# Kernel optimization log

Hardware: AMD Instinct MI355X
Metric: run time of the kernel (lower is better)

## Reference

```python
import jax, jax.numpy as jnp
import numpy as np

B = 65536          # batch
E = 512            # embedding_dim
SL = 128           # speed_latent_dim
H = 256            # hidden_size
NB = 6             # num_branch
D = E + SL         # 640, branch input dim


def _linear_init(k, din, dout):
    bound = 1.0 / np.sqrt(din)
    kw, kb = jax.random.split(k)
    W = jax.random.uniform(kw, (din, dout), minval=-bound, maxval=bound, dtype=jnp.float32)
    b = jax.random.uniform(kb, (dout,), minval=-bound, maxval=bound, dtype=jnp.float32)
    return W, b


def setup_inputs() -> dict:
    key = jax.random.key(0)
    ks = jax.random.split(key, 10)
    embedding = jax.random.normal(ks[0], (B, E), dtype=jnp.float32)
    speed = jax.random.uniform(ks[1], (B, 1), dtype=jnp.float32)
    command = jax.random.randint(ks[2], (B,), 1, NB + 1)  # values in 1..6

    # speed_in: Linear(1,H) -> ReLU -> Linear(H,SL)
    si_W1, si_b1 = _linear_init(ks[3], 1, H)
    si_W2, si_b2 = _linear_init(ks[4], H, SL)

    # speed_out: Linear(D,H) -> ReLU -> Linear(H,H) -> ReLU -> Linear(H,1)
    so_W1, so_b1 = _linear_init(ks[5], D, H)
    so_W2, so_b2 = _linear_init(ks[6], H, H)
    so_W3, so_b3 = _linear_init(ks[7], H, 1)

    # NB branches, each Linear(D,H)->ReLU->Linear(H,H)->ReLU->Linear(H,3)->Sigmoid
    def mk_branch(k):
        k1, k2, k3 = jax.random.split(k, 3)
        W1, b1 = _linear_init(k1, D, H)
        W2, b2 = _linear_init(k2, H, H)
        W3, b3 = _linear_init(k3, H, 3)
        return W1, b1, W2, b2, W3, b3

    bW1, bb1, bW2, bb2, bW3, bb3 = jax.vmap(mk_branch)(jax.random.split(ks[8], NB))

    return {
        "embedding": embedding, "speed": speed, "command": command,
        "si_W1": si_W1, "si_b1": si_b1, "si_W2": si_W2, "si_b2": si_b2,
        "bW1": bW1, "bb1": bb1, "bW2": bW2, "bb2": bb2, "bW3": bW3, "bb3": bb3,
        "so_W1": so_W1, "so_b1": so_b1, "so_W2": so_W2, "so_b2": so_b2,
        "so_W3": so_W3, "so_b3": so_b3,
    }


def reference(embedding, speed, command,
              si_W1, si_b1, si_W2, si_b2,
              bW1, bb1, bW2, bb2, bW3, bb3,
              so_W1, so_b1, so_W2, so_b2, so_W3, so_b3):
    # speed_in MLP and concat
    s = jax.nn.relu(speed @ si_W1 + si_b1) @ si_W2 + si_b2          # [B, SL]
    emb = jnp.concatenate([embedding, s], axis=1)                    # [B, D]

    # all branches computed densely (as in the torch module), then one-hot mask
    h1 = jax.nn.relu(jnp.einsum('bd,ndh->nbh', emb, bW1) + bb1[:, None, :])   # [NB,B,H]
    h2 = jax.nn.relu(jnp.einsum('nbh,nhk->nbk', h1, bW2) + bb2[:, None, :])   # [NB,B,H]
    out = jax.nn.sigmoid(jnp.einsum('nbk,nko->nbo', h2, bW3) + bb3[:, None, :])  # [NB,B,3]

    mask = (jnp.arange(NB)[:, None] == (command - 1)[None, :]).astype(out.dtype)  # [NB,B]
    control_pred = jnp.sum(out * mask[:, :, None], axis=0)           # [B, 3]

    # speed prediction head
    sp = jax.nn.relu(emb @ so_W1 + so_b1)
    sp = jax.nn.relu(sp @ so_W2 + so_b2)
    speed_pred = sp @ so_W3 + so_b3                                  # [B, 1]

    return control_pred, speed_pred
```

## Files before the change

### kernel.cpp

```cpp
#include <hip/hip_runtime.h>
#include <cstdint>
#include <cstddef>

typedef _Float16 f16;
typedef f16 f16x8 __attribute__((ext_vector_type(8)));
typedef float f32x4 __attribute__((ext_vector_type(4)));

#define B_ROWS 65536
#define NT_BRANCH 1030
#define NT_SPEED 1024

constexpr size_t OFF_SF16   = 0;
constexpr size_t SZ_SF16    = (size_t)B_ROWS * 128 * 2;
constexpr size_t OFF_SIW2T  = OFF_SF16 + SZ_SF16;
constexpr size_t SZ_SIW2T   = (size_t)128 * 256 * 2;
constexpr size_t OFF_BW1T   = OFF_SIW2T + SZ_SIW2T;
constexpr size_t SZ_BW1T    = (size_t)6 * 256 * 640 * 2;
constexpr size_t OFF_BW2T   = OFF_BW1T + SZ_BW1T;
constexpr size_t SZ_BW2T    = (size_t)6 * 256 * 256 * 2;
constexpr size_t OFF_SOW1T  = OFF_BW2T + SZ_BW2T;
constexpr size_t SZ_SOW1T   = (size_t)256 * 640 * 2;
constexpr size_t OFF_SOW2T  = OFF_SOW1T + SZ_SOW1T;
constexpr size_t SZ_SOW2T   = (size_t)256 * 256 * 2;
constexpr size_t OFF_COUNTS = OFF_SOW2T + SZ_SOW2T;
constexpr size_t OFF_CURSORS= OFF_COUNTS + 256;
constexpr size_t OFF_BINBASE= OFF_CURSORS + 256;
constexpr size_t OFF_TILECMD= OFF_BINBASE + 256;
constexpr size_t OFF_PERM   = OFF_TILECMD + 4352;
constexpr size_t WS_NEEDED  = OFF_PERM + (size_t)NT_BRANCH * 64 * 4;

__global__ void prep_kernel(const float* __restrict__ siW2,
                            const float* __restrict__ bW1,
                            const float* __restrict__ bW2,
                            const float* __restrict__ soW1,
                            const float* __restrict__ soW2,
                            f16* __restrict__ siW2T, f16* __restrict__ bW1T,
                            f16* __restrict__ bW2T, f16* __restrict__ soW1T,
                            f16* __restrict__ soW2T,
                            int* __restrict__ counts, int* __restrict__ cursors,
                            int* __restrict__ perm)
{
    const int bx = blockIdx.x;
    const int tx = threadIdx.x, ty = threadIdx.y;
    if (bx >= 1600) {
        const int tid = ty * 32 + tx;
        const int ib = bx - 1600;
        const int idx = ib * 256 + tid;
        if (idx < NT_BRANCH * 64) perm[idx] = -1;
        if (ib == 0 && tid < 6) { counts[tid] = 0; cursors[tid] = 0; }
        return;
    }
    const float* in; f16* out; int R, C, lb;
    if (bx < 960)       { int m = bx / 160;        lb = bx - m * 160;      in = bW1 + (size_t)m * 640 * 256; out = bW1T + (size_t)m * 640 * 256; R = 640; C = 256; }
    else if (bx < 1344) { int m = (bx - 960) / 64; lb = (bx - 960) - m * 64; in = bW2 + (size_t)m * 256 * 256; out = bW2T + (size_t)m * 256 * 256; R = 256; C = 256; }
    else if (bx < 1504) { lb = bx - 1344; in = soW1; out = soW1T; R = 640; C = 256; }
    else if (bx < 1568) { lb = bx - 1504; in = soW2; out = soW2T; R = 256; C = 256; }
    else                { lb = bx - 1568; in = siW2; out = siW2T; R = 256; C = 128; }
    const int txt = C >> 5;
    const int c0 = (lb % txt) << 5;
    const int r0 = (lb / txt) << 5;
    __shared__ float tile[32][33];
    #pragma unroll
    for (int i = 0; i < 4; ++i)
        tile[tx][ty + 8 * i] = in[(size_t)(r0 + ty + 8 * i) * C + c0 + tx];
    __syncthreads();
    #pragma unroll
    for (int i = 0; i < 4; ++i)
        out[(size_t)(c0 + ty + 8 * i) * R + r0 + tx] = (f16)tile[ty + 8 * i][tx];
}

__global__ __launch_bounds__(256) void speedin_kernel(
    const float* __restrict__ speed,
    const float* __restrict__ siW1, const float* __restrict__ sib1,
    const f16* __restrict__ siW2T, const float* __restrict__ sib2,
    f16* __restrict__ sF16)
{
    __shared__ f16 H[64 * 264];
    __shared__ float spd[64];
    const int tid = threadIdx.x;
    const int rb = blockIdx.x * 64;
    if (tid < 64) spd[tid] = speed[rb + tid];
    __syncthreads();
    {
        const float w1 = siW1[tid];
        const float b1v = sib1[tid];
        #pragma unroll 4
        for (int r = 0; r < 64; ++r) {
            float h = spd[r] * w1 + b1v;
            H[r * 264 + tid] = (f16)(h > 0.f ? h : 0.f);
        }
    }
    __syncthreads();
    const int w = tid >> 6, lane = tid & 63, lq = lane >> 4, l16 = lane & 15;
    const int nb = w * 32;
    f32x4 acc[4][2];
    #pragma unroll
    for (int mt = 0; mt < 4; ++mt)
        #pragma unroll
        for (int nt = 0; nt < 2; ++nt)
            acc[mt][nt] = (f32x4){0.f, 0.f, 0.f, 0.f};
    for (int ks = 0; ks < 8; ++ks) {
        const int koff = ks * 32 + lq * 8;
        f16x8 af[4], bf[2];
        #pragma unroll
        for (int mt = 0; mt < 4; ++mt)
            af[mt] = *(const f16x8*)(&H[(mt * 16 + l16) * 264 + koff]);
        #pragma unroll
        for (int nt = 0; nt < 2; ++nt)
            bf[nt] = *(const f16x8*)(siW2T + (size_t)(nb + nt * 16 + l16) * 256 + koff);
        #pragma unroll
        for (int mt = 0; mt < 4; ++mt)
            #pragma unroll
            for (int nt = 0; nt < 2; ++nt)
                acc[mt][nt] = __builtin_amdgcn_mfma_f32_16x16x32_f16(af[mt], bf[nt], acc[mt][nt], 0, 0, 0);
    }
    #pragma unroll
    for (int mt = 0; mt < 4; ++mt)
        #pragma unroll
        for (int nt = 0; nt < 2; ++nt) {
            const int n = nb + nt * 16 + l16;
            const float bv = sib2[n];
            #pragma unroll
            for (int r2 = 0; r2 < 4; ++r2) {
                const int m = mt * 16 + lq * 4 + r2;
                sF16[(size_t)(rb + m) * 128 + n] = (f16)(acc[mt][nt][r2] + bv);
            }
        }
}

__global__ void hist_kernel(const int* __restrict__ cmd, int* __restrict__ counts) {
    __shared__ int h[6];
    const int tid = threadIdx.x;
    if (tid < 6) h[tid] = 0;
    __syncthreads();
    const int i = blockIdx.x * 256 + tid;
    atomicAdd(&h[cmd[i] - 1], 1);
    __syncthreads();
    if (tid < 6) atomicAdd(&counts[tid], h[tid]);
}

__global__ void plan_kernel(const int* __restrict__ counts,
                            int* __restrict__ binBase, int* __restrict__ tile_cmd) {
    if (threadIdx.x == 0 && blockIdx.x == 0) {
        int base = 0, t = 0;
        for (int c = 0; c < 6; ++c) {
            binBase[c] = base;
            const int nt = (counts[c] + 63) >> 6;
            for (int j = 0; j < nt; ++j) tile_cmd[t++] = c;
            base += nt << 6;
        }
        binBase[6] = base;
        while (t < NT_BRANCH) tile_cmd[t++] = -1;
    }
}

__global__ void place_kernel(const int* __restrict__ cmd,
                             const int* __restrict__ binBase,
                             int* __restrict__ cursors, int* __restrict__ perm) {
    __shared__ int lcnt[6], lbase[6];
    const int tid = threadIdx.x;
    if (tid < 6) lcnt[tid] = 0;
    __syncthreads();
    const int i = blockIdx.x * 256 + tid;
    const int c = cmd[i] - 1;
    const int myr = atomicAdd(&lcnt[c], 1);
    __syncthreads();
    if (tid < 6) lbase[tid] = atomicAdd(&cursors[tid], lcnt[tid]);
    __syncthreads();
    perm[binBase[c] + lbase[c] + myr] = i;
}

__global__ __launch_bounds__(256, 2) void heads_kernel(
    const float* __restrict__ emb,
    const f16* __restrict__ sF16,
    const int* __restrict__ perm,
    const int* __restrict__ tile_cmd,
    const f16* __restrict__ bW1T, const f16* __restrict__ bW2T,
    const float* __restrict__ bW3,
    const float* __restrict__ bb1, const float* __restrict__ bb2,
    const float* __restrict__ bb3,
    const f16* __restrict__ soW1T, const f16* __restrict__ soW2T,
    const float* __restrict__ soW3,
    const float* __restrict__ sob1, const float* __restrict__ sob2,
    const float* __restrict__ sob3,
    float* __restrict__ out)
{
    __shared__ f16 lds[64 * 264];
    __shared__ int rowIdx[64];
    const int bx = blockIdx.x;
    const int tid = threadIdx.x;
    const bool is_speed = (bx >= NT_BRANCH);
    const f16 *W1T, *W2T;
    const float *W3, *bias1, *bias2, *bias3;
    if (is_speed) {
        const int t = bx - NT_BRANCH;
        if (tid < 64) rowIdx[tid] = t * 64 + tid;
        W1T = soW1T; W2T = soW2T; W3 = soW3;
        bias1 = sob1; bias2 = sob2; bias3 = sob3;
    } else {
        const int c = tile_cmd[bx];
        if (c < 0) return;
        if (tid < 64) rowIdx[tid] = perm[bx * 64 + tid];
        W1T = bW1T + (size_t)c * 256 * 640;
        W2T = bW2T + (size_t)c * 256 * 256;
        W3  = bW3  + (size_t)c * 256 * 3;
        bias1 = bb1 + c * 256; bias2 = bb2 + c * 256; bias3 = bb3 + c * 3;
    }
    const int w = tid >> 6, lane = tid & 63, lq = lane >> 4, l16 = lane & 15;
    const int nb = w * 64;
    f32x4 acc[4][4];
    #pragma unroll
    for (int mt = 0; mt < 4; ++mt)
        #pragma unroll
        for (int nt = 0; nt < 4; ++nt)
            acc[mt][nt] = (f32x4){0.f, 0.f, 0.f, 0.f};

    for (int kc = 0; kc < 10; ++kc) {
        __syncthreads();
        #pragma unroll
        for (int s = tid; s < 512; s += 256) {
            const int r = s >> 3, g = s & 7;
            int grow = rowIdx[r]; if (grow < 0) grow = 0;
            const int k0 = kc * 64 + g * 8;
            f16x8 v;
            if (k0 < 512) {
                const float* src = emb + (size_t)grow * 512 + k0;
                const float4 p0 = *(const float4*)(src);
                const float4 p1 = *(const float4*)(src + 4);
                v[0] = (f16)p0.x; v[1] = (f16)p0.y; v[2] = (f16)p0.z; v[3] = (f16)p0.w;
                v[4] = (f16)p1.x; v[5] = (f16)p1.y; v[6] = (f16)p1.z; v[7] = (f16)p1.w;
            } else {
                v = *(const f16x8*)(sF16 + (size_t)grow * 128 + (k0 - 512));
            }
            *(f16x8*)(&lds[r * 72 + g * 8]) = v;
        }
        __syncthreads();
        for (int ks = 0; ks < 2; ++ks) {
            const int koff = ks * 32 + lq * 8;
            f16x8 af[4], bf[4];
            #pragma unroll
            for (int mt = 0; mt < 4; ++mt)
                af[mt] = *(const f16x8*)(&lds[(mt * 16 + l16) * 72 + koff]);
            #pragma unroll
            for (int nt = 0; nt < 4; ++nt)
                bf[nt] = *(const f16x8*)(W1T + (size_t)(nb + nt * 16 + l16) * 640 + kc * 64 + koff);
            #pragma unroll
            for (int mt = 0; mt < 4; ++mt)
                #pragma unroll
                for (int nt = 0; nt < 4; ++nt)
                    acc[mt][nt] = __builtin_amdgcn_mfma_f32_16x16x32_f16(af[mt], bf[nt], acc[mt][nt], 0, 0, 0);
        }
    }
    __syncthreads();
    #pragma unroll
    for (int mt = 0; mt < 4; ++mt)
        #pragma unroll
        for (int nt = 0; nt < 4; ++nt) {
            const int n = nb + nt * 16 + l16;
            const float bv = bias1[n];
            #pragma unroll
            for (int r2 = 0; r2 < 4; ++r2) {
                const int m = mt * 16 + lq * 4 + r2;
                const float v = acc[mt][nt][r2] + bv;
                lds[m * 264 + n] = (f16)(v > 0.f ? v : 0.f);
            }
            acc[mt][nt] = (f32x4){0.f, 0.f, 0.f, 0.f};
        }
    __syncthreads();
    for (int ks = 0; ks < 8; ++ks) {
        const int koff = ks * 32 + lq * 8;
        f16x8 af[4], bf[4];
        #pragma unroll
        for (int mt = 0; mt < 4; ++mt)
            af[mt] = *(const f16x8*)(&lds[(mt * 16 + l16) * 264 + koff]);
        #pragma unroll
        for (int nt = 0; nt < 4; ++nt)
            bf[nt] = *(const f16x8*)(W2T + (size_t)(nb + nt * 16 + l16) * 256 + koff);
        #pragma unroll
        for (int mt = 0; mt < 4; ++mt)
            #pragma unroll
            for (int nt = 0; nt < 4; ++nt)
                acc[mt][nt] = __builtin_amdgcn_mfma_f32_16x16x32_f16(af[mt], bf[nt], acc[mt][nt], 0, 0, 0);
    }
    __syncthreads();
    #pragma unroll
    for (int mt = 0; mt < 4; ++mt)
        #pragma unroll
        for (int nt = 0; nt < 4; ++nt) {
            const int n = nb + nt * 16 + l16;
            const float bv = bias2[n];
            #pragma unroll
            for (int r2 = 0; r2 < 4; ++r2) {
                const int m = mt * 16 + lq * 4 + r2;
                const float v = acc[mt][nt][r2] + bv;
                lds[m * 264 + n] = (f16)(v > 0.f ? v : 0.f);
            }
        }
    __syncthreads();
    const int r = tid >> 2, p = tid & 3;
    const int grow = rowIdx[r];
    if (!is_speed) {
        float a0 = 0.f, a1 = 0.f, a2 = 0.f;
        #pragma unroll 8
        for (int kk = 0; kk < 64; ++kk) {
            const int k = p * 64 + kk;
            const float h = (float)lds[r * 264 + k];
            a0 += h * W3[k * 3 + 0];
            a1 += h * W3[k * 3 + 1];
            a2 += h * W3[k * 3 + 2];
        }
        a0 += __shfl_xor(a0, 1); a0 += __shfl_xor(a0, 2);
        a1 += __shfl_xor(a1, 1); a1 += __shfl_xor(a1, 2);
        a2 += __shfl_xor(a2, 1); a2 += __shfl_xor(a2, 2);
        if (p == 0 && grow >= 0) {
            out[(size_t)grow * 3 + 0] = 1.f / (1.f + __expf(-(a0 + bias3[0])));
            out[(size_t)grow * 3 + 1] = 1.f / (1.f + __expf(-(a1 + bias3[1])));
            out[(size_t)grow * 3 + 2] = 1.f / (1.f + __expf(-(a2 + bias3[2])));
        }
    } else {
        float a0 = 0.f;
        #pragma unroll 8
        for (int kk = 0; kk < 64; ++kk) {
            const int k = p * 64 + kk;
            a0 += (float)lds[r * 264 + k] * W3[k];
        }
        a0 += __shfl_xor(a0, 1); a0 += __shfl_xor(a0, 2);
        if (p == 0) out[(size_t)3 * B_ROWS + grow] = a0 + bias3[0];
    }
}

extern "C" void kernel_launch(void* const* d_in, const int* in_sizes, int n_in,
                              void* d_out, int out_size, void* d_ws, size_t ws_size,
                              hipStream_t stream) {
    (void)in_sizes; (void)n_in; (void)out_size; (void)ws_size;
    const float* embedding = (const float*)d_in[0];
    const float* speed     = (const float*)d_in[1];
    const int*   command   = (const int*)d_in[2];
    const float* si_W1 = (const float*)d_in[3];
    const float* si_b1 = (const float*)d_in[4];
    const float* si_W2 = (const float*)d_in[5];
    const float* si_b2 = (const float*)d_in[6];
    const float* bW1   = (const float*)d_in[7];
    const float* bb1   = (const float*)d_in[8];
    const float* bW2   = (const float*)d_in[9];
    const float* bb2   = (const float*)d_in[10];
    const float* bW3   = (const float*)d_in[11];
    const float* bb3   = (const float*)d_in[12];
    const float* so_W1 = (const float*)d_in[13];
    const float* so_b1 = (const float*)d_in[14];
    const float* so_W2 = (const float*)d_in[15];
    const float* so_b2 = (const float*)d_in[16];
    const float* so_W3 = (const float*)d_in[17];
    const float* so_b3 = (const float*)d_in[18];
    float* out = (float*)d_out;

    char* ws = (char*)d_ws;
    f16* sF16   = (f16*)(ws + OFF_SF16);
    f16* siW2T  = (f16*)(ws + OFF_SIW2T);
    f16* bW1T   = (f16*)(ws + OFF_BW1T);
    f16* bW2T   = (f16*)(ws + OFF_BW2T);
    f16* soW1T  = (f16*)(ws + OFF_SOW1T);
    f16* soW2T  = (f16*)(ws + OFF_SOW2T);
    int* counts = (int*)(ws + OFF_COUNTS);
    int* cursors= (int*)(ws + OFF_CURSORS);
    int* binBase= (int*)(ws + OFF_BINBASE);
    int* tile_cmd = (int*)(ws + OFF_TILECMD);
    int* perm   = (int*)(ws + OFF_PERM);

    prep_kernel<<<1858, dim3(32, 8), 0, stream>>>(
        si_W2, bW1, bW2, so_W1, so_W2,
        siW2T, bW1T, bW2T, soW1T, soW2T, counts, cursors, perm);
    speedin_kernel<<<1024, 256, 0, stream>>>(speed, si_W1, si_b1, siW2T, si_b2, sF16);
    hist_kernel<<<256, 256, 0, stream>>>(command, counts);
    plan_kernel<<<1, 64, 0, stream>>>(counts, binBase, tile_cmd);
    place_kernel<<<256, 256, 0, stream>>>(command, binBase, cursors, perm);
    heads_kernel<<<NT_BRANCH + NT_SPEED, 256, 0, stream>>>(
        embedding, sF16, perm, tile_cmd,
        bW1T, bW2T, bW3, bb1, bb2, bb3,
        soW1T, soW2T, so_W3, so_b1, so_b2, so_b3, out);
}
```

Baseline: 414.8 us.

## Pre-pack fp16 concatenated input and stream layer-1 operands from global memory

```diff
diff --git a/kernel.cpp b/kernel.cpp
--- a/kernel.cpp
+++ b/kernel.cpp
@@ -10,9 +10,9 @@
 #define NT_BRANCH 1030
 #define NT_SPEED 1024
 
-constexpr size_t OFF_SF16   = 0;
-constexpr size_t SZ_SF16    = (size_t)B_ROWS * 128 * 2;
-constexpr size_t OFF_SIW2T  = OFF_SF16 + SZ_SF16;
+constexpr size_t OFF_EMBF16 = 0;
+constexpr size_t SZ_EMBF16  = (size_t)B_ROWS * 640 * 2;
+constexpr size_t OFF_SIW2T  = OFF_EMBF16 + SZ_EMBF16;
 constexpr size_t SZ_SIW2T   = (size_t)128 * 256 * 2;
 constexpr size_t OFF_BW1T   = OFF_SIW2T + SZ_SIW2T;
 constexpr size_t SZ_BW1T    = (size_t)6 * 256 * 640 * 2;
@@ -22,7 +22,11 @@
 constexpr size_t SZ_SOW1T   = (size_t)256 * 640 * 2;
 constexpr size_t OFF_SOW2T  = OFF_SOW1T + SZ_SOW1T;
 constexpr size_t SZ_SOW2T   = (size_t)256 * 256 * 2;
-constexpr size_t OFF_COUNTS = OFF_SOW2T + SZ_SOW2T;
+constexpr size_t OFF_BW3T16 = OFF_SOW2T + SZ_SOW2T;
+constexpr size_t SZ_BW3T16  = (size_t)6 * 16 * 256 * 2;
+constexpr size_t OFF_SOW3T16= OFF_BW3T16 + SZ_BW3T16;
+constexpr size_t SZ_SOW3T16 = (size_t)16 * 256 * 2;
+constexpr size_t OFF_COUNTS = OFF_SOW3T16 + SZ_SOW3T16;
 constexpr size_t OFF_CURSORS= OFF_COUNTS + 256;
 constexpr size_t OFF_BINBASE= OFF_CURSORS + 256;
 constexpr size_t OFF_TILECMD= OFF_BINBASE + 256;
@@ -34,24 +38,38 @@
                             const float* __restrict__ bW2,
                             const float* __restrict__ soW1,
                             const float* __restrict__ soW2,
+                            const float* __restrict__ bW3,
+                            const float* __restrict__ soW3,
                             f16* __restrict__ siW2T, f16* __restrict__ bW1T,
                             f16* __restrict__ bW2T, f16* __restrict__ soW1T,
                             f16* __restrict__ soW2T,
+                            f16* __restrict__ bW3T16, f16* __restrict__ soW3T16,
                             int* __restrict__ counts, int* __restrict__ cursors,
                             int* __restrict__ perm)
 {
     const int bx = blockIdx.x;
     const int tx = threadIdx.x, ty = threadIdx.y;
-    if (bx >= 1600) {
-        const int tid = ty * 32 + tx;
-        const int ib = bx - 1600;
+    const int tid = ty * 32 + tx;
+    if (bx >= 1601) {
+        const int ib = bx - 1601;
         const int idx = ib * 256 + tid;
         if (idx < NT_BRANCH * 64) perm[idx] = -1;
         if (ib == 0 && tid < 6) { counts[tid] = 0; cursors[tid] = 0; }
         return;
     }
+    if (bx == 1600) {
+        for (int i = tid; i < 6 * 16 * 256; i += 256) {
+            const int c = i >> 12, rem = i & 4095, n = rem >> 8, k = rem & 255;
+            bW3T16[i] = (n < 3) ? (f16)bW3[((size_t)c * 256 + k) * 3 + n] : (f16)0;
+        }
+        for (int i = tid; i < 16 * 256; i += 256) {
+            const int n = i >> 8, k = i & 255;
+            soW3T16[i] = (n == 0) ? (f16)soW3[k] : (f16)0;
+        }
+        return;
+    }
     const float* in; f16* out; int R, C, lb;
-    if (bx < 960)       { int m = bx / 160;        lb = bx - m * 160;      in = bW1 + (size_t)m * 640 * 256; out = bW1T + (size_t)m * 640 * 256; R = 640; C = 256; }
+    if (bx < 960)       { int m = bx / 160;        lb = bx - m * 160;       in = bW1 + (size_t)m * 640 * 256; out = bW1T + (size_t)m * 640 * 256; R = 640; C = 256; }
     else if (bx < 1344) { int m = (bx - 960) / 64; lb = (bx - 960) - m * 64; in = bW2 + (size_t)m * 256 * 256; out = bW2T + (size_t)m * 256 * 256; R = 256; C = 256; }
     else if (bx < 1504) { lb = bx - 1344; in = soW1; out = soW1T; R = 640; C = 256; }
     else if (bx < 1568) { lb = bx - 1504; in = soW2; out = soW2T; R = 256; C = 256; }
@@ -69,26 +87,44 @@
         out[(size_t)(c0 + ty + 8 * i) * R + r0 + tx] = (f16)tile[ty + 8 * i][tx];
 }
 
-__global__ __launch_bounds__(256) void speedin_kernel(
-    const float* __restrict__ speed,
+__global__ __launch_bounds__(256) void pack_kernel(
+    const float* __restrict__ emb, const float* __restrict__ speed,
     const float* __restrict__ siW1, const float* __restrict__ sib1,
     const f16* __restrict__ siW2T, const float* __restrict__ sib2,
-    f16* __restrict__ sF16)
+    const int* __restrict__ cmd,
+    f16* __restrict__ embF16, int* __restrict__ counts)
 {
     __shared__ f16 H[64 * 264];
     __shared__ float spd[64];
+    __shared__ int h[6];
     const int tid = threadIdx.x;
     const int rb = blockIdx.x * 64;
-    if (tid < 64) spd[tid] = speed[rb + tid];
-    __syncthreads();
+    if (tid < 6) h[tid] = 0;
+    __syncthreads();
+    if (tid < 64) {
+        spd[tid] = speed[rb + tid];
+        atomicAdd(&h[cmd[rb + tid] - 1], 1);
+    }
+    __syncthreads();
+    if (tid < 6 && h[tid] > 0) atomicAdd(&counts[tid], h[tid]);
     {
-        const float w1 = siW1[tid];
-        const float b1v = sib1[tid];
+        const float w1 = siW1[tid], b1v = sib1[tid];
         #pragma unroll 4
         for (int r = 0; r < 64; ++r) {
-            float h = spd[r] * w1 + b1v;
-            H[r * 264 + tid] = (f16)(h > 0.f ? h : 0.f);
-        }
+            float hv = spd[r] * w1 + b1v;
+            H[r * 264 + tid] = (f16)(hv > 0.f ? hv : 0.f);
+        }
+    }
+    #pragma unroll
+    for (int i = tid; i < 4096; i += 256) {
+        const int r = i >> 6, c8 = (i & 63) << 3;
+        const float* src = emb + (size_t)(rb + r) * 512 + c8;
+        const float4 p0 = *(const float4*)(src);
+        const float4 p1 = *(const float4*)(src + 4);
+        f16x8 v;
+        v[0] = (f16)p0.x; v[1] = (f16)p0.y; v[2] = (f16)p0.z; v[3] = (f16)p0.w;
+        v[4] = (f16)p1.x; v[5] = (f16)p1.y; v[6] = (f16)p1.z; v[7] = (f16)p1.w;
+        *(f16x8*)(embF16 + (size_t)(rb + r) * 640 + c8) = v;
     }
     __syncthreads();
     const int w = tid >> 6, lane = tid & 63, lq = lane >> 4, l16 = lane & 15;
@@ -123,34 +159,32 @@
             #pragma unroll
             for (int r2 = 0; r2 < 4; ++r2) {
                 const int m = mt * 16 + lq * 4 + r2;
-                sF16[(size_t)(rb + m) * 128 + n] = (f16)(acc[mt][nt][r2] + bv);
+                embF16[(size_t)(rb + m) * 640 + 512 + n] = (f16)(acc[mt][nt][r2] + bv);
             }
         }
-}
-
-__global__ void hist_kernel(const int* __restrict__ cmd, int* __restrict__ counts) {
-    __shared__ int h[6];
-    const int tid = threadIdx.x;
-    if (tid < 6) h[tid] = 0;
-    __syncthreads();
-    const int i = blockIdx.x * 256 + tid;
-    atomicAdd(&h[cmd[i] - 1], 1);
-    __syncthreads();
-    if (tid < 6) atomicAdd(&counts[tid], h[tid]);
 }
 
 __global__ void plan_kernel(const int* __restrict__ counts,
                             int* __restrict__ binBase, int* __restrict__ tile_cmd) {
-    if (threadIdx.x == 0 && blockIdx.x == 0) {
-        int base = 0, t = 0;
+    __shared__ int tbase[7];
+    if (threadIdx.x == 0) {
+        int base = 0, tb = 0;
         for (int c = 0; c < 6; ++c) {
             binBase[c] = base;
+            tbase[c] = tb;
             const int nt = (counts[c] + 63) >> 6;
-            for (int j = 0; j < nt; ++j) tile_cmd[t++] = c;
+            tb += nt;
             base += nt << 6;
         }
-        binBase[6] = base;
-        while (t < NT_BRANCH) tile_cmd[t++] = -1;
+        tbase[6] = tb;
+    }
+    __syncthreads();
+    for (int t = threadIdx.x; t < NT_BRANCH; t += 256) {
+        int c = -1;
+        #pragma unroll
+        for (int j = 0; j < 6; ++j)
+            if (t >= tbase[j] && t < tbase[j + 1]) c = j;
+        tile_cmd[t] = c;
     }
 }
 
@@ -170,17 +204,15 @@
     perm[binBase[c] + lbase[c] + myr] = i;
 }
 
-__global__ __launch_bounds__(256, 2) void heads_kernel(
-    const float* __restrict__ emb,
-    const f16* __restrict__ sF16,
-    const int* __restrict__ perm,
-    const int* __restrict__ tile_cmd,
+__global__ __launch_bounds__(256, 3) void heads_kernel(
+    const f16* __restrict__ embF16,
+    const int* __restrict__ perm, const int* __restrict__ tile_cmd,
     const f16* __restrict__ bW1T, const f16* __restrict__ bW2T,
-    const float* __restrict__ bW3,
+    const f16* __restrict__ bW3T16,
     const float* __restrict__ bb1, const float* __restrict__ bb2,
     const float* __restrict__ bb3,
     const f16* __restrict__ soW1T, const f16* __restrict__ soW2T,
-    const float* __restrict__ soW3,
+    const f16* __restrict__ soW3T16,
     const float* __restrict__ sob1, const float* __restrict__ sob2,
     const float* __restrict__ sob3,
     float* __restrict__ out)
@@ -190,12 +222,12 @@
     const int bx = blockIdx.x;
     const int tid = threadIdx.x;
     const bool is_speed = (bx >= NT_BRANCH);
-    const f16 *W1T, *W2T;
-    const float *W3, *bias1, *bias2, *bias3;
+    const f16 *W1T, *W2T, *W3T;
+    const float *bias1, *bias2, *bias3;
     if (is_speed) {
         const int t = bx - NT_BRANCH;
         if (tid < 64) rowIdx[tid] = t * 64 + tid;
-        W1T = soW1T; W2T = soW2T; W3 = soW3;
+        W1T = soW1T; W2T = soW2T; W3T = soW3T16;
         bias1 = sob1; bias2 = sob2; bias3 = sob3;
     } else {
         const int c = tile_cmd[bx];
@@ -203,11 +235,23 @@
         if (tid < 64) rowIdx[tid] = perm[bx * 64 + tid];
         W1T = bW1T + (size_t)c * 256 * 640;
         W2T = bW2T + (size_t)c * 256 * 256;
-        W3  = bW3  + (size_t)c * 256 * 3;
+        W3T = bW3T16 + (size_t)c * 16 * 256;
         bias1 = bb1 + c * 256; bias2 = bb2 + c * 256; bias3 = bb3 + c * 3;
     }
+    __syncthreads();
     const int w = tid >> 6, lane = tid & 63, lq = lane >> 4, l16 = lane & 15;
     const int nb = w * 64;
+    const f16* arow[4];
+    #pragma unroll
+    for (int mt = 0; mt < 4; ++mt) {
+        const int g = rowIdx[mt * 16 + l16];
+        arow[mt] = embF16 + (size_t)(g < 0 ? 0 : g) * 640;
+    }
+    const f16* brow[4];
+    #pragma unroll
+    for (int nt = 0; nt < 4; ++nt)
+        brow[nt] = W1T + (size_t)(nb + nt * 16 + l16) * 640;
+
     f32x4 acc[4][4];
     #pragma unroll
     for (int mt = 0; mt < 4; ++mt)
@@ -215,117 +259,147 @@
         for (int nt = 0; nt < 4; ++nt)
             acc[mt][nt] = (f32x4){0.f, 0.f, 0.f, 0.f};
 
-    for (int kc = 0; kc < 10; ++kc) {
-        __syncthreads();
-        #pragma unroll
-        for (int s = tid; s < 512; s += 256) {
-            const int r = s >> 3, g = s & 7;
-            int grow = rowIdx[r]; if (grow < 0) grow = 0;
-            const int k0 = kc * 64 + g * 8;
-            f16x8 v;
-            if (k0 < 512) {
-                const float* src = emb + (size_t)grow * 512 + k0;
-                const float4 p0 = *(const float4*)(src);
-                const float4 p1 = *(const float4*)(src + 4);
-                v[0] = (f16)p0.x; v[1] = (f16)p0.y; v[2] = (f16)p0.z; v[3] = (f16)p0.w;
-                v[4] = (f16)p1.x; v[5] = (f16)p1.y; v[6] = (f16)p1.z; v[7] = (f16)p1.w;
-            } else {
-                v = *(const f16x8*)(sF16 + (size_t)grow * 128 + (k0 - 512));
+    f16x8 a0[4], b0[4], a1[4], b1[4];
+    {
+        const int k = lq * 8;
+        #pragma unroll
+        for (int mt = 0; mt < 4; ++mt) a0[mt] = *(const f16x8*)(arow[mt] + k);
+        #pragma unroll
+        for (int nt = 0; nt < 4; ++nt) b0[nt] = *(const f16x8*)(brow[nt] + k);
+    }
+    for (int kp = 0; kp < 10; ++kp) {
+        {
+            const int k = kp * 64 + 32 + lq * 8;
+            #pragma unroll
+            for (int mt = 0; mt < 4; ++mt) a1[mt] = *(const f16x8*)(arow[mt] + k);
+            #pragma unroll
+            for (int nt = 0; nt < 4; ++nt) b1[nt] = *(const f16x8*)(brow[nt] + k);
+        }
+        #pragma unroll
+        for (int mt = 0; mt < 4; ++mt)
+            #pragma unroll
+            for (int nt = 0; nt < 4; ++nt)
+                acc[mt][nt] = __builtin_amdgcn_mfma_f32_16x16x32_f16(a0[mt], b0[nt], acc[mt][nt], 0, 0, 0);
+        if (kp < 9) {
+            const int k = (kp + 1) * 64 + lq * 8;
+            #pragma unroll
+            for (int mt = 0; mt < 4; ++mt) a0[mt] = *(const f16x8*)(arow[mt] + k);
+            #pragma unroll
+            for (int nt = 0; nt < 4; ++nt) b0[nt] = *(const f16x8*)(brow[nt] + k);
+        }
+        #pragma unroll
+        for (int mt = 0; mt < 4; ++mt)
+            #pragma unroll
+            for (int nt = 0; nt < 4; ++nt)
+                acc[mt][nt] = __builtin_amdgcn_mfma_f32_16x16x32_f16(a1[mt], b1[nt], acc[mt][nt], 0, 0, 0);
+    }
+    float b1r[4];
+    #pragma unroll
+    for (int nt = 0; nt < 4; ++nt) b1r[nt] = bias1[nb + nt * 16 + l16];
+    #pragma unroll
+    for (int mt = 0; mt < 4; ++mt)
+        #pragma unroll
+        for (int nt = 0; nt < 4; ++nt) {
+            const int n = nb + nt * 16 + l16;
+            #pragma unroll
+            for (int r2 = 0; r2 < 4; ++r2) {
+                const int m = mt * 16 + lq * 4 + r2;
+                const float v = acc[mt][nt][r2] + b1r[nt];
+                lds[m * 264 + n] = (f16)(v > 0.f ? v : 0.f);
             }
-            *(f16x8*)(&lds[r * 72 + g * 8]) = v;
-        }
-        __syncthreads();
-        for (int ks = 0; ks < 2; ++ks) {
-            const int koff = ks * 32 + lq * 8;
-            f16x8 af[4], bf[4];
+            acc[mt][nt] = (f32x4){0.f, 0.f, 0.f, 0.f};
+        }
+    __syncthreads();
+    const f16* brow2[4];
+    #pragma unroll
+    for (int nt = 0; nt < 4; ++nt)
+        brow2[nt] = W2T + (size_t)(nb + nt * 16 + l16) * 256;
+    f16x8 c0[4], c1[4];
+    {
+        const int k = lq * 8;
+        #pragma unroll
+        for (int nt = 0; nt < 4; ++nt) c0[nt] = *(const f16x8*)(brow2[nt] + k);
+    }
+    for (int kp = 0; kp < 4; ++kp) {
+        {
+            const int k = kp * 64 + 32 + lq * 8;
+            #pragma unroll
+            for (int nt = 0; nt < 4; ++nt) c1[nt] = *(const f16x8*)(brow2[nt] + k);
+        }
+        {
+            const int koff = kp * 64 + lq * 8;
+            f16x8 af[4];
             #pragma unroll
             for (int mt = 0; mt < 4; ++mt)
-                af[mt] = *(const f16x8*)(&lds[(mt * 16 + l16) * 72 + koff]);
-            #pragma unroll
-            for (int nt = 0; nt < 4; ++nt)
-                bf[nt] = *(const f16x8*)(W1T + (size_t)(nb + nt * 16 + l16) * 640 + kc * 64 + koff);
+                af[mt] = *(const f16x8*)(&lds[(mt * 16 + l16) * 264 + koff]);
             #pragma unroll
             for (int mt = 0; mt < 4; ++mt)
                 #pragma unroll
                 for (int nt = 0; nt < 4; ++nt)
-                    acc[mt][nt] = __builtin_amdgcn_mfma_f32_16x16x32_f16(af[mt], bf[nt], acc[mt][nt], 0, 0, 0);
-        }
-    }
+                    acc[mt][nt] = __builtin_amdgcn_mfma_f32_16x16x32_f16(af[mt], c0[nt], acc[mt][nt], 0, 0, 0);
+        }
+        if (kp < 3) {
+            const int k = (kp + 1) * 64 + lq * 8;
+            #pragma unroll
+            for (int nt = 0; nt < 4; ++nt) c0[nt] = *(const f16x8*)(brow2[nt] + k);
+        }
+        {
+            const int koff = kp * 64 + 32 + lq * 8;
+            f16x8 af[4];
+            #pragma unroll
+            for (int mt = 0; mt < 4; ++mt)
+                af[mt] = *(const f16x8*)(&lds[(mt * 16 + l16) * 264 + koff]);
+            #pragma unroll
+            for (int mt = 0; mt < 4; ++mt)
+                #pragma unroll
+                for (int nt = 0; nt < 4; ++nt)
+                    acc[mt][nt] = __builtin_amdgcn_mfma_f32_16x16x32_f16(af[mt], c1[nt], acc[mt][nt], 0, 0, 0);
+        }
+    }
+    float b2r[4];
+    #pragma unroll
+    for (int nt = 0; nt < 4; ++nt) b2r[nt] = bias2[nb + nt * 16 + l16];
     __syncthreads();
     #pragma unroll
     for (int mt = 0; mt < 4; ++mt)
         #pragma unroll
         for (int nt = 0; nt < 4; ++nt) {
             const int n = nb + nt * 16 + l16;
-            const float bv = bias1[n];
             #pragma unroll
             for (int r2 = 0; r2 < 4; ++r2) {
                 const int m = mt * 16 + lq * 4 + r2;
-                const float v = acc[mt][nt][r2] + bv;
+                const float v = acc[mt][nt][r2] + b2r[nt];
                 lds[m * 264 + n] = (f16)(v > 0.f ? v : 0.f);
             }
-            acc[mt][nt] = (f32x4){0.f, 0.f, 0.f, 0.f};
-        }
-    __syncthreads();
+        }
+    __syncthreads();
+    f32x4 acc3 = (f32x4){0.f, 0.f, 0.f, 0.f};
+    const f16* w3row = W3T + (size_t)l16 * 256;
+    #pragma unroll
     for (int ks = 0; ks < 8; ++ks) {
         const int koff = ks * 32 + lq * 8;
-        f16x8 af[4], bf[4];
-        #pragma unroll
-        for (int mt = 0; mt < 4; ++mt)
-            af[mt] = *(const f16x8*)(&lds[(mt * 16 + l16) * 264 + koff]);
-        #pragma unroll
-        for (int nt = 0; nt < 4; ++nt)
-            bf[nt] = *(const f16x8*)(W2T + (size_t)(nb + nt * 16 + l16) * 256 + koff);
-        #pragma unroll
-        for (int mt = 0; mt < 4; ++mt)
-            #pragma unroll
-            for (int nt = 0; nt < 4; ++nt)
-                acc[mt][nt] = __builtin_amdgcn_mfma_f32_16x16x32_f16(af[mt], bf[nt], acc[mt][nt], 0, 0, 0);
-    }
-    __syncthreads();
-    #pragma unroll
-    for (int mt = 0; mt < 4; ++mt)
-        #pragma unroll
-        for (int nt = 0; nt < 4; ++nt) {
-            const int n = nb + nt * 16 + l16;
-            const float bv = bias2[n];
+        const f16x8 af = *(const f16x8*)(&lds[(w * 16 + l16) * 264 + koff]);
+        const f16x8 bf = *(const f16x8*)(w3row + koff);
+        acc3 = __builtin_amdgcn_mfma_f32_16x16x32_f16(af, bf, acc3, 0, 0, 0);
+    }
+    const int orow = w * 16 + lq * 4;
+    if (!is_speed) {
+        if (l16 < 3) {
+            const float b3 = bias3[l16];
             #pragma unroll
             for (int r2 = 0; r2 < 4; ++r2) {
-                const int m = mt * 16 + lq * 4 + r2;
-                const float v = acc[mt][nt][r2] + bv;
-                lds[m * 264 + n] = (f16)(v > 0.f ? v : 0.f);
+                const int g = rowIdx[orow + r2];
+                if (g >= 0)
+                    out[(size_t)g * 3 + l16] = 1.f / (1.f + __expf(-(acc3[r2] + b3)));
             }
         }
-    __syncthreads();
-    const int r = tid >> 2, p = tid & 3;
-    const int grow = rowIdx[r];
-    if (!is_speed) {
-        float a0 = 0.f, a1 = 0.f, a2 = 0.f;
-        #pragma unroll 8
-        for (int kk = 0; kk < 64; ++kk) {
-            const int k = p * 64 + kk;
-            const float h = (float)lds[r * 264 + k];
-            a0 += h * W3[k * 3 + 0];
-            a1 += h * W3[k * 3 + 1];
-            a2 += h * W3[k * 3 + 2];
-        }
-        a0 += __shfl_xor(a0, 1); a0 += __shfl_xor(a0, 2);
-        a1 += __shfl_xor(a1, 1); a1 += __shfl_xor(a1, 2);
-        a2 += __shfl_xor(a2, 1); a2 += __shfl_xor(a2, 2);
-        if (p == 0 && grow >= 0) {
-            out[(size_t)grow * 3 + 0] = 1.f / (1.f + __expf(-(a0 + bias3[0])));
-            out[(size_t)grow * 3 + 1] = 1.f / (1.f + __expf(-(a1 + bias3[1])));
-            out[(size_t)grow * 3 + 2] = 1.f / (1.f + __expf(-(a2 + bias3[2])));
-        }
     } else {
-        float a0 = 0.f;
-        #pragma unroll 8
-        for (int kk = 0; kk < 64; ++kk) {
-            const int k = p * 64 + kk;
-            a0 += (float)lds[r * 264 + k] * W3[k];
-        }
-        a0 += __shfl_xor(a0, 1); a0 += __shfl_xor(a0, 2);
-        if (p == 0) out[(size_t)3 * B_ROWS + grow] = a0 + bias3[0];
+        if (l16 == 0) {
+            const float b3 = bias3[0];
+            #pragma unroll
+            for (int r2 = 0; r2 < 4; ++r2)
+                out[(size_t)3 * B_ROWS + rowIdx[orow + r2]] = acc3[r2] + b3;
+        }
     }
 }
 
@@ -355,27 +429,30 @@
     float* out = (float*)d_out;
 
     char* ws = (char*)d_ws;
-    f16* sF16   = (f16*)(ws + OFF_SF16);
+    f16* embF16 = (f16*)(ws + OFF_EMBF16);
     f16* siW2T  = (f16*)(ws + OFF_SIW2T);
     f16* bW1T   = (f16*)(ws + OFF_BW1T);
     f16* bW2T   = (f16*)(ws + OFF_BW2T);
     f16* soW1T  = (f16*)(ws + OFF_SOW1T);
     f16* soW2T  = (f16*)(ws + OFF_SOW2T);
+    f16* bW3T16 = (f16*)(ws + OFF_BW3T16);
+    f16* soW3T16= (f16*)(ws + OFF_SOW3T16);
     int* counts = (int*)(ws + OFF_COUNTS);
     int* cursors= (int*)(ws + OFF_CURSORS);
     int* binBase= (int*)(ws + OFF_BINBASE);
     int* tile_cmd = (int*)(ws + OFF_TILECMD);
     int* perm   = (int*)(ws + OFF_PERM);
 
-    prep_kernel<<<1858, dim3(32, 8), 0, stream>>>(
-        si_W2, bW1, bW2, so_W1, so_W2,
-        siW2T, bW1T, bW2T, soW1T, soW2T, counts, cursors, perm);
-    speedin_kernel<<<1024, 256, 0, stream>>>(speed, si_W1, si_b1, siW2T, si_b2, sF16);
-    hist_kernel<<<256, 256, 0, stream>>>(command, counts);
-    plan_kernel<<<1, 64, 0, stream>>>(counts, binBase, tile_cmd);
+    prep_kernel<<<1859, dim3(32, 8), 0, stream>>>(
+        si_W2, bW1, bW2, so_W1, so_W2, bW3, so_W3,
+        siW2T, bW1T, bW2T, soW1T, soW2T, bW3T16, soW3T16,
+        counts, cursors, perm);
+    pack_kernel<<<1024, 256, 0, stream>>>(
+        embedding, speed, si_W1, si_b1, siW2T, si_b2, command, embF16, counts);
+    plan_kernel<<<1, 256, 0, stream>>>(counts, binBase, tile_cmd);
     place_kernel<<<256, 256, 0, stream>>>(command, binBase, cursors, perm);
     heads_kernel<<<NT_BRANCH + NT_SPEED, 256, 0, stream>>>(
-        embedding, sF16, perm, tile_cmd,
-        bW1T, bW2T, bW3, bb1, bb2, bb3,
-        soW1T, soW2T, so_W3, so_b1, so_b2, so_b3, out);
-}
+        embF16, perm, tile_cmd,
+        bW1T, bW2T, bW3T16, bb1, bb2, bb3,
+        soW1T, soW2T, soW3T16, so_b1, so_b2, so_b3, out);
+}
```

Result: slower. 475.5 us (+14.6%).
